# Kernel optimization log

Measured on AMD Instinct MI355X. Metric: run time of the kernel, lower is better.

## Reference

```python
import jax, jax.numpy as jnp
import numpy as np

NBIT = 8
NSPLIT = 255.0  # 2**NBIT - 1


def _quantized_matmul(x, w_clean, eps):
    # Faithful port of quantization(): bit-slice x into NBIT binary planes, run a
    # noisy linear per plane with weight w + randn*|w|*0.1, and sum. The 8
    # sequential fc() calls are fused into one einsum over the bit axis.
    # x: (..., in); w_clean: (out, in); eps: (NBIT, out, in) standard normal.
    mn = jnp.min(x)
    mx = jnp.max(x)
    q = ((x - mn) / (mx - mn) * NSPLIT).astype(jnp.uint8).astype(jnp.int32)  # truncating cast as in torch
    quant_base = 2 ** jnp.arange(NBIT, dtype=jnp.int32)
    binary = ((q[..., None] & quant_base) != 0).astype(x.dtype)              # (..., in, NBIT)
    scaled = binary * (2.0 ** jnp.arange(NBIT)).astype(x.dtype)              # plane i scaled by 2**i
    w_noisy = w_clean[None] + eps * jnp.abs(w_clean)[None] * 0.1             # (NBIT, out, in)
    z = jnp.einsum('...ib,boi->...o', scaled, w_noisy)
    return z, mn, mx, w_noisy[-1]  # fc.weight after loop == last noisy weight


def _forward(node_embedding, edge_embedding, nbr_mask, cond1, cond2, eps1, eps2, bn_gamma, bn_beta):
    B, At, Nbr, Fe = edge_embedding.shape
    Fn = node_embedding.shape[-1]
    c1 = jnp.concatenate(
        [jnp.broadcast_to(node_embedding[:, :, None, :], (B, At, Nbr, Fn)), edge_embedding],
        axis=3)                                                              # (B, At, Nbr, Fn+Fe)
    # quantization + re_quantization through fc (re-quant uses last noisy fc.weight)
    z1, mn1, mx1, w_last = _quantized_matmul(c1, cond1[0], eps1)
    bias1 = jnp.sum(mn1 * w_last, axis=1)                                    # (H1,)
    h = jax.nn.relu(z1 / NSPLIT * (mx1 - mn1) + bias1)                       # (B, At, Nbr, H1)
    # quantization + re_quantization through fc_2 (re-quant uses conductance[1][-1])
    z2, mn2, mx2, _ = _quantized_matmul(h, cond2[0], eps2)
    bias2 = jnp.sum(mn2 * cond2[-1], axis=1)                                 # (2*Fn,)
    c2 = z2 / NSPLIT * (mx2 - mn2) + bias2                                   # (B, At, Nbr, 2*Fn)
    nbr_gate, nbr_extract = jnp.split(c2, 2, axis=3)
    nbr_sumed = jax.nn.sigmoid(nbr_gate) * jnp.tanh(nbr_extract) * nbr_mask[..., None]
    nbr_sumed = jnp.sum(nbr_sumed, axis=2)                                   # (B, At, Fn)
    # BatchNorm1d in training mode: batch statistics over flattened (B*At)
    flat = nbr_sumed.reshape(-1, Fn)
    mean = jnp.mean(flat, axis=0)
    var = jnp.var(flat, axis=0)  # biased variance, as torch BN uses for normalization
    bn = ((flat - mean) / jnp.sqrt(var + 1e-5) * bn_gamma + bn_beta).reshape(B, At, Fn)
    return jax.nn.relu(node_embedding + bn)


def setup_inputs() -> dict:
    key = jax.random.key(0)
    ks = jax.random.split(key, 7)
    B, At, Nbr, Fn, Fe = 16, 96, 12, 64, 64
    H1, H2 = 4 * (Fn + Fe), 2 * Fn
    return {
        'node_embedding': jax.random.normal(ks[0], (B, At, Fn), jnp.float32),
        'edge_embedding': jax.random.normal(ks[1], (B, At, Nbr, Fe), jnp.float32),
        'nbr_mask': (jax.random.uniform(ks[2], (B, At, Nbr)) > 0.5).astype(jnp.float32),
        'cond1': jax.random.normal(ks[3], (2, H1, Fn + Fe), jnp.float32) * 0.05,
        'cond2': jax.random.normal(ks[4], (2, H2, H1), jnp.float32) * 0.05,
        'eps1': jax.random.normal(ks[5], (NBIT, H1, Fn + Fe), jnp.float32),
        'eps2': jax.random.normal(ks[6], (NBIT, H2, H1), jnp.float32),
        'bn_gamma': jnp.ones((Fn,), jnp.float32),
        'bn_beta': jnp.zeros((Fn,), jnp.float32),
    }


def reference(node_embedding, edge_embedding, nbr_mask, cond1, cond2, eps1, eps2, bn_gamma, bn_beta):
    return _forward(node_embedding, edge_embedding, nbr_mask, cond1, cond2, eps1, eps2, bn_gamma, bn_beta)
```

## Files before the change

kernel.cpp:

```cpp
#include <hip/hip_runtime.h>
#include <stdint.h>

#define B_    16
#define AT_   96
#define NBR_  12
#define FN_   64
#define FE_   64
#define M1    (B_*AT_*NBR_)
#define R_    (B_*AT_)
#define K1Q   128
#define N1    512
#define K2Q   512
#define N2    128
#define SPLIT2 4

typedef _Float16 f16x8 __attribute__((ext_vector_type(8)));
typedef float    f32x4 __attribute__((ext_vector_type(4)));
typedef __attribute__((address_space(1))) const void gconst_void;
typedef __attribute__((address_space(3))) void lds_void;

#define OFF_SCAL  0u
#define OFF_B1R   256u
#define OFF_B2R   (OFF_B1R + 2048u)
#define OFF_Q1    4096u
#define OFF_W1E   (OFF_Q1  + (size_t)M1*K1Q)
#define OFF_W2E   (OFF_W1E + (size_t)N1*K1Q*8*2)
#define OFF_Q2    (OFF_W2E + (size_t)N2*K2Q*8*2)
#define OFF_H     (OFF_Q2  + (size_t)M1*K2Q)
#define OFF_ZP    OFF_H
#define OFF_NS    (OFF_H   + (size_t)M1*N1*4)

__device__ __forceinline__ unsigned int enc_f(float f) {
    unsigned int u = __float_as_uint(f);
    return (u & 0x80000000u) ? ~u : (u | 0x80000000u);
}
__device__ __forceinline__ float dec_f(unsigned int u) {
    return __uint_as_float((u & 0x80000000u) ? (u & 0x7FFFFFFFu) : ~u);
}

__global__ void k_init(unsigned int* scal, float* b1raw, float* b2raw) {
    int t = threadIdx.x;
    if (t == 0) { scal[0] = 0xFFFFFFFFu; scal[1] = 0u; scal[2] = 0xFFFFFFFFu; scal[3] = 0u; }
    if (t < N1) b1raw[t] = 0.f;
    if (t < N2) b2raw[t] = 0.f;
}

__global__ __launch_bounds__(256) void k_minmax_c1(const float* __restrict__ node,
                                                   const float* __restrict__ edge,
                                                   unsigned int* __restrict__ scal) {
    const int nn = B_*AT_*FN_;
    const int ntot = nn + M1*FE_;
    float mn = 3.0e38f, mx = -3.0e38f;
    for (int idx = blockIdx.x*blockDim.x + threadIdx.x; idx < ntot; idx += gridDim.x*blockDim.x) {
        float x = (idx < nn) ? node[idx] : edge[idx - nn];
        mn = fminf(mn, x); mx = fmaxf(mx, x);
    }
    __shared__ float smn[256], smx[256];
    smn[threadIdx.x] = mn; smx[threadIdx.x] = mx; __syncthreads();
    for (int s = 128; s > 0; s >>= 1) {
        if (threadIdx.x < s) {
            smn[threadIdx.x] = fminf(smn[threadIdx.x], smn[threadIdx.x+s]);
            smx[threadIdx.x] = fmaxf(smx[threadIdx.x], smx[threadIdx.x+s]);
        }
        __syncthreads();
    }
    if (threadIdx.x == 0) { atomicMin(&scal[0], enc_f(smn[0])); atomicMax(&scal[1], enc_f(smx[0])); }
}

template<int KQ, int N, int SBASE, bool USE_SECOND>
__global__ __launch_bounds__(256) void k_prep_w16(const float* __restrict__ w_clean,
                                                  const float* __restrict__ eps,
                                                  const unsigned int* __restrict__ scal,
                                                  float* __restrict__ braw,
                                                  _Float16* __restrict__ We) {
    int idx = blockIdx.x*blockDim.x + threadIdx.x;
    if (idx >= N*KQ) return;
    int o = idx / KQ;
    int i = idx % KQ;
    float mn = dec_f(scal[SBASE]), mx = dec_f(scal[SBASE+1]);
    float s = (mx - mn) * (1.0f/255.0f);
    float w = w_clean[idx];
    float aw = fabsf(w) * 0.1f;
    union { _Float16 h[8]; uint4 u; } pk;
    float p = s;
    float v7 = 0.f;
    #pragma unroll
    for (int b = 0; b < 8; b++) {
        float e = eps[(size_t)b*N*KQ + idx];
        float v = w + e*aw;
        if (b == 7) v7 = v;
        pk.h[b] = (_Float16)(v * p);
        p *= 2.0f;
    }
    *(uint4*)&We[((size_t)o*KQ + i)*8] = pk.u;
    float bv = USE_SECOND ? w_clean[(size_t)N*KQ + idx] : v7;
    #pragma unroll
    for (int off = 32; off > 0; off >>= 1) bv += __shfl_down(bv, off);
    if ((threadIdx.x & 63) == 0) atomicAdd(&braw[o], bv);
}

__global__ __launch_bounds__(256) void k_quant_c1(const float* __restrict__ node,
                                                  const float* __restrict__ edge,
                                                  const unsigned int* __restrict__ scal,
                                                  unsigned int* __restrict__ q1) {
    int idx = blockIdx.x*256 + threadIdx.x;
    int m = idx >> 5, dw = idx & 31;
    const float mn = dec_f(scal[0]), rng = dec_f(scal[1]) - mn;
    float4 x;
    if (dw < 16) x = *(const float4*)&node[(m/NBR_)*FN_ + dw*4];
    else         x = *(const float4*)&edge[(size_t)m*FE_ + (dw-16)*4];
    unsigned int b0 = (unsigned char)(int)((x.x - mn) / rng * 255.0f);
    unsigned int b1 = (unsigned char)(int)((x.y - mn) / rng * 255.0f);
    unsigned int b2 = (unsigned char)(int)((x.z - mn) / rng * 255.0f);
    unsigned int b3 = (unsigned char)(int)((x.w - mn) / rng * 255.0f);
    q1[idx] = b0 | (b1 << 8) | (b2 << 16) | (b3 << 24);
}

__global__ __launch_bounds__(256) void k_quant_h(const float* __restrict__ h,
                                                 const unsigned int* __restrict__ scal,
                                                 unsigned int* __restrict__ q2) {
    int idx = blockIdx.x*256 + threadIdx.x;
    const float mn = dec_f(scal[2]), rng = dec_f(scal[3]) - mn;
    float4 x = *(const float4*)&h[(size_t)idx*4];
    unsigned int b0 = (unsigned char)(int)((x.x - mn) / rng * 255.0f);
    unsigned int b1 = (unsigned char)(int)((x.y - mn) / rng * 255.0f);
    unsigned int b2 = (unsigned char)(int)((x.z - mn) / rng * 255.0f);
    unsigned int b3 = (unsigned char)(int)((x.w - mn) / rng * 255.0f);
    q2[idx] = b0 | (b1 << 8) | (b2 << 16) | (b3 << 24);
}

__device__ __forceinline__ f16x8 expand_byte(unsigned int byte) {
    unsigned int r2 = byte | (byte << 15);
    union { unsigned int u[4]; f16x8 h; } t;
    t.u[0] = ( r2       & 0x00010001u) * 0x3C00u;
    t.u[1] = ((r2 >> 2) & 0x00010001u) * 0x3C00u;
    t.u[2] = ((r2 >> 4) & 0x00010001u) * 0x3C00u;
    t.u[3] = ((r2 >> 6) & 0x00010001u) * 0x3C00u;
    return t.h;
}

template<int KQ, int N, int SPLITK, bool EPI1>
__global__ __launch_bounds__(256, 4) void kg(const unsigned char* __restrict__ q,
                                             const _Float16* __restrict__ W,
                                             const float* __restrict__ braw,
                                             void* __restrict__ outv,
                                             unsigned int* __restrict__ scal) {
    constexpr int KP  = KQ * 8;
    constexpr int KPS = KP / SPLITK;
    __shared__ _Float16 Bs[8192];
    __shared__ uint2    Qs[256];

    const int tid  = threadIdx.x;
    const int lane = tid & 63;
    const int w    = tid >> 6;
    const int wm   = (w & 1) * 64;
    const int kg   = w >> 1;
    const int l15  = lane & 15;
    const int lq   = lane >> 4;
    const int sh8  = lq * 8;
    const int m0   = blockIdx.x * 128;
    const int o0   = blockIdx.y * 64;
    const int kbase = blockIdx.z * KPS;

    f32x4 acc[4][4] = {};

    const int akg = tid >> 7, agt = tid & 127;
    const unsigned char* aq = q + (size_t)(m0 + agt)*KQ + (kbase >> 3) + akg*64;

    #pragma unroll 1
    for (int it = 0; it < KPS/128; ++it) {
        __syncthreads();
        uint2 qa = *(const uint2*)(aq + it*8);
        #pragma unroll
        for (int iss = 0; iss < 4; ++iss) {
            int s    = iss*256 + tid;
            int skg  = s >> 9;
            int sg   = s & 511;
            int n    = sg >> 3;
            int csrc = (sg & 7) ^ (n & 7);
            const _Float16* gp = W + (size_t)(o0 + n)*KP + kbase + skg*512 + it*64 + csrc*8;
            _Float16* lp = &Bs[(size_t)(iss*256 + (tid & ~63)) * 8];
            __builtin_amdgcn_global_load_lds((gconst_void*)gp, (lds_void*)lp, 16, 0, 0);
        }
        Qs[(akg << 7) + agt] = qa;
        __builtin_amdgcn_s_waitcnt(0);
        __syncthreads();

        uint2 qd[4];
        #pragma unroll
        for (int mf = 0; mf < 4; ++mf)
            qd[mf] = Qs[kg*128 + wm + mf*16 + l15];
        #pragma unroll
        for (int kf = 0; kf < 2; ++kf) {
            f16x8 bf[4];
            #pragma unroll
            for (int nf = 0; nf < 4; ++nf) {
                const int nl = nf*16 + l15;
                const int ch = kf*4 + lq;
                bf[nf] = *(const f16x8*)&Bs[kg*4096 + nl*64 + ((ch ^ (nl & 7)) << 3)];
            }
            #pragma unroll
            for (int mf = 0; mf < 4; ++mf) {
                unsigned int byte = ((kf ? qd[mf].y : qd[mf].x) >> sh8) & 0xFFu;
                f16x8 a = expand_byte(byte);
                #pragma unroll
                for (int nf = 0; nf < 4; ++nf)
                    acc[mf][nf] = __builtin_amdgcn_mfma_f32_16x16x32_f16(a, bf[nf], acc[mf][nf], 0, 0, 0);
            }
        }
    }

    float* red = (float*)Bs;
    #pragma unroll
    for (int nf = 0; nf < 4; ++nf) {
        __syncthreads();
        if (kg == 1) {
            #pragma unroll
            for (int mf = 0; mf < 4; ++mf)
                *(f32x4*)&red[(w & 1)*1024 + mf*256 + lane*4] = acc[mf][nf];
        }
        __syncthreads();
        if (kg == 0) {
            #pragma unroll
            for (int mf = 0; mf < 4; ++mf)
                acc[mf][nf] += *(const f32x4*)&red[(w & 1)*1024 + mf*256 + lane*4];
        }
    }

    if (EPI1) {
        float tmn = 3.0e38f, tmx = -3.0e38f;
        if (kg == 0) {
            float* out = (float*)outv;
            const float mn1 = dec_f(scal[0]);
            float bv[4];
            #pragma unroll
            for (int nf = 0; nf < 4; ++nf) bv[nf] = mn1 * braw[o0 + nf*16 + l15];
            #pragma unroll
            for (int mf = 0; mf < 4; ++mf) {
                const int mr = m0 + wm + mf*16 + lq*4;
                #pragma unroll
                for (int nf = 0; nf < 4; ++nf) {
                    const int oc = o0 + nf*16 + l15;
                    #pragma unroll
                    for (int r = 0; r < 4; ++r) {
                        float v = acc[mf][nf][r] + bv[nf];
                        v = fmaxf(v, 0.0f);
                        tmn = fminf(tmn, v); tmx = fmaxf(tmx, v);
                        out[(size_t)(mr + r)*N + oc] = v;
                    }
                }
            }
        }
        __syncthreads();
        red[tid] = tmn; red[256 + tid] = tmx;
        __syncthreads();
        for (int s = 128; s > 0; s >>= 1) {
            if (tid < s) {
                red[tid]       = fminf(red[tid],       red[tid + s]);
                red[256 + tid] = fmaxf(red[256 + tid], red[256 + tid + s]);
            }
            __syncthreads();
        }
        if (tid == 0) { atomicMin(&scal[2], enc_f(red[0])); atomicMax(&scal[3], enc_f(red[256])); }
    } else {
        if (kg == 0) {
            _Float16* op = (_Float16*)outv + (size_t)blockIdx.z * ((size_t)M1 * N);
            #pragma unroll
            for (int mf = 0; mf < 4; ++mf) {
                const int mr = m0 + wm + mf*16 + lq*4;
                #pragma unroll
                for (int nf = 0; nf < 4; ++nf) {
                    const int oc = o0 + nf*16 + l15;
                    #pragma unroll
                    for (int r = 0; r < 4; ++r)
                        op[(size_t)(mr + r)*N + oc] = (_Float16)acc[mf][nf][r];
                }
            }
        }
    }
}

__global__ __launch_bounds__(256) void k_nbr(const _Float16* __restrict__ zp,
                                             const float* __restrict__ b2raw,
                                             const unsigned int* __restrict__ scal,
                                             const float* __restrict__ mask,
                                             float* __restrict__ ns) {
    const size_t SP = (size_t)M1 * N2;
    int tid = threadIdx.x;
    int r = blockIdx.x*4 + (tid >> 6);
    int f = tid & 63;
    const float mn2 = dec_f(scal[2]);
    float bg = mn2 * b2raw[f], be = mn2 * b2raw[64 + f];
    float s = 0.f;
    #pragma unroll
    for (int n = 0; n < NBR_; n++) {
        int m = r*NBR_ + n;
        size_t base = (size_t)m * N2;
        float g = bg, e = be;
        #pragma unroll
        for (int z = 0; z < SPLIT2; z++) {
            g += (float)zp[z*SP + base + f];
            e += (float)zp[z*SP + base + 64 + f];
        }
        float sig = 1.0f / (1.0f + expf(-g));
        s += sig * tanhf(e) * mask[m];
    }
    ns[r*64 + f] = s;
}

__global__ __launch_bounds__(256) void k_bn(const float* __restrict__ ns,
                                            const float* __restrict__ node,
                                            const float* __restrict__ gamma,
                                            const float* __restrict__ beta,
                                            float* __restrict__ out) {
    int f = blockIdx.x;
    int tid = threadIdx.x;
    float x[6];
    float s = 0.f, ss = 0.f;
    #pragma unroll
    for (int k = 0; k < 6; k++) {
        int r = tid + k*256;
        x[k] = ns[r*64 + f];
        s += x[k]; ss += x[k]*x[k];
    }
    __shared__ float rs[256], rss[256];
    rs[tid] = s; rss[tid] = ss; __syncthreads();
    for (int st = 128; st > 0; st >>= 1) {
        if (tid < st) { rs[tid] += rs[tid+st]; rss[tid] += rss[tid+st]; }
        __syncthreads();
    }
    float mean = rs[0] / 1536.0f;
    float var  = rss[0] / 1536.0f - mean*mean;
    float denom = sqrtf(var + 1e-5f);
    float g = gamma[f], bt = beta[f];
    #pragma unroll
    for (int k = 0; k < 6; k++) {
        int r = tid + k*256;
        float v = node[r*64 + f] + ((x[k] - mean) / denom * g + bt);
        out[r*64 + f] = fmaxf(v, 0.f);
    }
}

extern "C" void kernel_launch(void* const* d_in, const int* in_sizes, int n_in,
                              void* d_out, int out_size, void* d_ws, size_t ws_size,
                              hipStream_t stream) {
    const float* node  = (const float*)d_in[0];
    const float* edge  = (const float*)d_in[1];
    const float* mask  = (const float*)d_in[2];
    const float* cond1 = (const float*)d_in[3];
    const float* cond2 = (const float*)d_in[4];
    const float* eps1  = (const float*)d_in[5];
    const float* eps2  = (const float*)d_in[6];
    const float* gamma = (const float*)d_in[7];
    const float* beta  = (const float*)d_in[8];
    float* out = (float*)d_out;
    char* ws = (char*)d_ws;

    unsigned int*  scal = (unsigned int*)(ws + OFF_SCAL);
    float* b1raw = (float*)(ws + OFF_B1R);
    float* b2raw = (float*)(ws + OFF_B2R);
    unsigned char* q1 = (unsigned char*)(ws + OFF_Q1);
    _Float16* W1e = (_Float16*)(ws + OFF_W1E);
    _Float16* W2e = (_Float16*)(ws + OFF_W2E);
    unsigned char* q2 = (unsigned char*)(ws + OFF_Q2);
    float*    h  = (float*)(ws + OFF_H);
    _Float16* zp = (_Float16*)(ws + OFF_ZP);
    float*    ns = (float*)(ws + OFF_NS);

    k_init<<<1, 1024, 0, stream>>>(scal, b1raw, b2raw);
    k_minmax_c1<<<512, 256, 0, stream>>>(node, edge, scal);
    k_prep_w16<K1Q, N1, 0, false><<<(N1*K1Q + 255)/256, 256, 0, stream>>>(cond1, eps1, scal, b1raw, W1e);
    k_quant_c1<<<(M1*32)/256, 256, 0, stream>>>(node, edge, scal, (unsigned int*)q1);
    kg<K1Q, N1, 1, true><<<dim3(M1/128, N1/64, 1), 256, 0, stream>>>(q1, W1e, b1raw, h, scal);
    k_prep_w16<K2Q, N2, 2, true><<<(N2*K2Q + 255)/256, 256, 0, stream>>>(cond2, eps2, scal, b2raw, W2e);
    k_quant_h<<<(M1*128)/256, 256, 0, stream>>>(h, scal, (unsigned int*)q2);
    kg<K2Q, N2, SPLIT2, false><<<dim3(M1/128, N2/64, SPLIT2), 256, 0, stream>>>(q2, W2e, b2raw, zp, scal);
    k_nbr<<<R_/4, 256, 0, stream>>>(zp, b2raw, scal, mask, ns);
    k_bn<<<64, 256, 0, stream>>>(ns, node, gamma, beta, out);
}
```

Before: 198.5 us.

## Double-buffer LDS tiles and prefetch next K-slice during MFMA compute

```diff
diff --git a/kernel.cpp b/kernel.cpp
--- a/kernel.cpp
+++ b/kernel.cpp
@@ -147,8 +147,9 @@
                                              unsigned int* __restrict__ scal) {
     constexpr int KP  = KQ * 8;
     constexpr int KPS = KP / SPLITK;
-    __shared__ _Float16 Bs[8192];
-    __shared__ uint2    Qs[256];
+    constexpr int NIT = KPS / 128;
+    __shared__ _Float16 Bs[16384];
+    __shared__ uint2    Qs[512];
 
     const int tid  = threadIdx.x;
     const int lane = tid & 63;
@@ -164,32 +165,42 @@
 
     f32x4 acc[4][4] = {};
 
-    const int akg = tid >> 7, agt = tid & 127;
-    const unsigned char* aq = q + (size_t)(m0 + agt)*KQ + (kbase >> 3) + akg*64;
-
-    #pragma unroll 1
-    for (int it = 0; it < KPS/128; ++it) {
-        __syncthreads();
-        uint2 qa = *(const uint2*)(aq + it*8);
+    unsigned int bo[4];
+    #pragma unroll
+    for (int iss = 0; iss < 4; ++iss) {
+        int s = iss*256 + tid, skg = s >> 9, sg = s & 511, n = sg >> 3;
+        int csrc = (sg & 7) ^ (n & 7);
+        bo[iss] = (unsigned int)((o0 + n)*KP + kbase + skg*512 + csrc*8);
+    }
+    const int bdl = (tid & ~63) * 8;
+
+    unsigned int ao[2];
+    #pragma unroll
+    for (int i = 0; i < 2; ++i) {
+        int d = w*128 + i*64 + lane;
+        int kga = d >> 8, row = (d >> 1) & 127, half = d & 1;
+        ao[i] = (unsigned int)((m0 + row)*KQ + (kbase >> 3) + kga*64 + half*4);
+    }
+    const int adl = w * 512;
+
+    auto stage = [&](int IT, int BUF) {
         #pragma unroll
-        for (int iss = 0; iss < 4; ++iss) {
-            int s    = iss*256 + tid;
-            int skg  = s >> 9;
-            int sg   = s & 511;
-            int n    = sg >> 3;
-            int csrc = (sg & 7) ^ (n & 7);
-            const _Float16* gp = W + (size_t)(o0 + n)*KP + kbase + skg*512 + it*64 + csrc*8;
-            _Float16* lp = &Bs[(size_t)(iss*256 + (tid & ~63)) * 8];
-            __builtin_amdgcn_global_load_lds((gconst_void*)gp, (lds_void*)lp, 16, 0, 0);
-        }
-        Qs[(akg << 7) + agt] = qa;
-        __builtin_amdgcn_s_waitcnt(0);
-        __syncthreads();
-
+        for (int iss = 0; iss < 4; ++iss)
+            __builtin_amdgcn_global_load_lds((gconst_void*)(W + bo[iss] + IT*64),
+                (lds_void*)(Bs + BUF*8192 + iss*2048 + bdl), 16, 0, 0);
+        #pragma unroll
+        for (int i = 0; i < 2; ++i)
+            __builtin_amdgcn_global_load_lds((gconst_void*)(q + ao[i] + IT*8),
+                (lds_void*)((char*)Qs + BUF*2048 + i*256 + adl), 4, 0, 0);
+    };
+
+    auto compute = [&](int cur) {
+        const _Float16* Bc = Bs + cur*8192 + kg*4096;
+        const uint2*    Qc = Qs + cur*256 + kg*128;
         uint2 qd[4];
         #pragma unroll
         for (int mf = 0; mf < 4; ++mf)
-            qd[mf] = Qs[kg*128 + wm + mf*16 + l15];
+            qd[mf] = Qc[wm + mf*16 + l15];
         #pragma unroll
         for (int kf = 0; kf < 2; ++kf) {
             f16x8 bf[4];
@@ -197,7 +208,7 @@
             for (int nf = 0; nf < 4; ++nf) {
                 const int nl = nf*16 + l15;
                 const int ch = kf*4 + lq;
-                bf[nf] = *(const f16x8*)&Bs[kg*4096 + nl*64 + ((ch ^ (nl & 7)) << 3)];
+                bf[nf] = *(const f16x8*)&Bc[nl*64 + ((ch ^ (nl & 7)) << 3)];
             }
             #pragma unroll
             for (int mf = 0; mf < 4; ++mf) {
@@ -208,7 +219,22 @@
                     acc[mf][nf] = __builtin_amdgcn_mfma_f32_16x16x32_f16(a, bf[nf], acc[mf][nf], 0, 0, 0);
             }
         }
-    }
+    };
+
+    stage(0, 0);
+    #pragma unroll 1
+    for (int it = 0; it < NIT-1; ++it) {
+        const int cur = it & 1;
+        stage(it+1, cur ^ 1);
+        asm volatile("s_waitcnt vmcnt(6)" ::: "memory");
+        asm volatile("s_barrier" ::: "memory");
+        compute(cur);
+        asm volatile("s_waitcnt lgkmcnt(0)" ::: "memory");
+        asm volatile("s_barrier" ::: "memory");
+    }
+    asm volatile("s_waitcnt vmcnt(0)" ::: "memory");
+    asm volatile("s_barrier" ::: "memory");
+    compute((NIT-1) & 1);
 
     float* red = (float*)Bs;
     #pragma unroll
```

Result: no change. 201.4 us (+1.5%).
